# Performance work log

Measured on AMD Instinct MI355X. Metric: run time of the kernel, lower is better.

## Reference

```python
import jax, jax.numpy as jnp
import numpy as np
import math

N, E, IN, HID, HEADS, OUT, G = 20000, 320000, 128, 32, 8, 10, 16


def _conv(x, src, dst, wq, bq, wk, bk, wv, bv, ws, bs, heads):
    # PyG TransformerConv (concat=True, root_weight=True, eval mode)
    n = x.shape[0]
    c = wq.shape[1] // heads
    q = (x @ wq + bq).reshape(n, heads, c)[dst]   # [E, H, C] query at dst
    k = (x @ wk + bk).reshape(n, heads, c)[src]   # [E, H, C] key at src
    v = (x @ wv + bv).reshape(n, heads, c)[src]   # [E, H, C] value at src
    a = (q * k).sum(-1) / math.sqrt(c)            # [E, H] per-edge scores
    amax = jax.lax.stop_gradient(jax.ops.segment_max(a, dst, num_segments=n))
    a = jnp.exp(a - amax[dst])
    denom = jax.ops.segment_sum(a, dst, num_segments=n)
    a = a / (denom[dst] + 1e-16)                  # segment softmax over incoming edges
    agg = jax.ops.segment_sum(a[:, :, None] * v, dst, num_segments=n)  # [N, H, C]
    return agg.reshape(n, heads * c) + x @ ws + bs  # skip connection (lin_skip)


def setup_inputs() -> dict:
    key = jax.random.key(0)
    keys = iter(jax.random.split(key, 64))
    d = {}
    d["x"] = jax.random.normal(next(keys), (N, IN), jnp.float32)
    d["edge_index"] = jax.random.randint(next(keys), (2, E), 0, N)
    d["batch"] = jnp.sort(jax.random.randint(next(keys), (N,), 0, G))
    dims_in = [IN, HID * HEADS, HID * HEADS, HID * HEADS]
    heads_l = [HEADS, HEADS, HEADS, 1]
    for i in range(4):
        di, h = dims_in[i], heads_l[i]
        do = h * HID
        s = 1.0 / math.sqrt(di)
        for nm in ("wq", "wk", "wv", "ws"):
            d[f"{nm}{i}"] = jax.random.normal(next(keys), (di, do), jnp.float32) * s
        for nm in ("bq", "bk", "bv", "bs"):
            d[f"{nm}{i}"] = jnp.zeros((do,), jnp.float32)
    d["wlin"] = jax.random.normal(next(keys), (HID, OUT), jnp.float32) / math.sqrt(HID)
    d["blin"] = jnp.zeros((OUT,), jnp.float32)
    return d


def reference(x, edge_index, batch,
              wq0, bq0, wk0, bk0, wv0, bv0, ws0, bs0,
              wq1, bq1, wk1, bk1, wv1, bv1, ws1, bs1,
              wq2, bq2, wk2, bk2, wv2, bv2, ws2, bs2,
              wq3, bq3, wk3, bk3, wv3, bv3, ws3, bs3,
              wlin, blin):
    src, dst = edge_index[0], edge_index[1]
    layer_params = [
        (wq0, bq0, wk0, bk0, wv0, bv0, ws0, bs0, HEADS),
        (wq1, bq1, wk1, bk1, wv1, bv1, ws1, bs1, HEADS),
        (wq2, bq2, wk2, bk2, wv2, bv2, ws2, bs2, HEADS),
        (wq3, bq3, wk3, bk3, wv3, bv3, ws3, bs3, 1),
    ]
    h = x
    for p in layer_params:
        h = jax.nn.relu(_conv(h, src, dst, *p))  # dropout is identity in eval mode
    counts = jax.ops.segment_sum(jnp.ones((h.shape[0],), h.dtype), batch, num_segments=G)
    pooled = jax.ops.segment_sum(h, batch, num_segments=G) / jnp.maximum(counts, 1.0)[:, None]
    logits = pooled @ wlin + blin
    return jax.nn.log_softmax(logits, axis=-1)
```

## Files before the change

### kernel.cpp

```cpp
#include <hip/hip_runtime.h>
#include <hip/hip_fp16.h>
#include <math.h>

#define HID 32
#define GRP 16
#define OUTC 10

typedef __attribute__((ext_vector_type(8))) short short8;
typedef __attribute__((ext_vector_type(4))) float f32x4;

struct P4     { const float*  W[4]; const float* B[4]; float* C[4]; __half* kv; };
struct W4     { const float*  w[4]; };
struct PZmfma { const ushort* wh[4]; const ushort* wl[4]; const float* bias[4]; float* C[4]; __half* kv; };

__device__ __forceinline__ ushort f2bf(float f) {
    unsigned u = __float_as_uint(f);
    unsigned r = (u + 0x7FFFu + ((u >> 16) & 1u)) >> 16;
    return (ushort)r;
}
__device__ __forceinline__ float bf2f(ushort h) {
    return __uint_as_float(((unsigned)h) << 16);
}
__device__ __forceinline__ float2 h2f(unsigned u) {
    __half2 h = *reinterpret_cast<__half2*>(&u);
    return __half22float2(h);
}

__global__ void fill_i32(int* p, int v, int n) {
    int i = blockIdx.x * blockDim.x + threadIdx.x;
    if (i < n) p[i] = v;
}

__global__ void count_deg(const int* __restrict__ dst, int* __restrict__ deg, int E) {
    int e = blockIdx.x * blockDim.x + threadIdx.x;
    if (e < E) atomicAdd(&deg[dst[e]], 1);
}

__global__ __launch_bounds__(256) void scan_offsets(const int* __restrict__ deg,
                                                    int* __restrict__ offs,
                                                    int* __restrict__ pos, int n) {
    __shared__ int partial[256];
    const int t = threadIdx.x;
    const int chunk = (n + 255) / 256;
    const int start = t * chunk;
    const int end   = min(start + chunk, n);
    int sum = 0;
    for (int i = start; i < end; i++) sum += deg[i];
    partial[t] = sum;
    __syncthreads();
    for (int s = 1; s < 256; s <<= 1) {
        int v = (t >= s) ? partial[t - s] : 0;
        __syncthreads();
        partial[t] += v;
        __syncthreads();
    }
    int base = (t == 0) ? 0 : partial[t - 1];
    for (int i = start; i < end; i++) {
        offs[i] = base; pos[i] = base;
        base += deg[i];
    }
    if (t == 255) offs[n] = base;
}

__global__ void scatter_edges(const int* __restrict__ dst, int* __restrict__ pos,
                              int* __restrict__ perm, int E) {
    int e = blockIdx.x * blockDim.x + threadIdx.x;
    if (e < E) {
        int slot = atomicAdd(&pos[dst[e]], 1);
        perm[slot] = e;
    }
}

__global__ void gather_src(const int* __restrict__ perm, const int* __restrict__ src,
                           int* __restrict__ srcPerm, int E) {
    int i = blockIdx.x * blockDim.x + threadIdx.x;
    if (i < E) srcPerm[i] = src[perm[i]];
}

__global__ void split_f32(const float* __restrict__ x, ushort* __restrict__ hi,
                          ushort* __restrict__ lo, long long n) {
    long long i = (long long)blockIdx.x * blockDim.x + threadIdx.x;
    if (i >= n) return;
    float v = x[i];
    ushort h = f2bf(v);
    ushort l = f2bf(v - bf2f(h));
    hi[i] = h; lo[i] = l;
}

__global__ void splitT_w(W4 wp, ushort* __restrict__ wh, ushort* __restrict__ wl, int K) {
    const int NN = 256;
    int z = blockIdx.y;
    const float* W = wp.w[z];
    ushort* whz = wh + (size_t)z * K * NN;
    ushort* wlz = wl + (size_t)z * K * NN;
    int i = blockIdx.x * blockDim.x + threadIdx.x;
    if (i >= K * NN) return;
    int k = i / NN, n = i - k * NN;
    float v = W[i];
    ushort h = f2bf(v);
    ushort l = f2bf(v - bf2f(h));
    whz[(size_t)n * K + k] = h;
    wlz[(size_t)n * K + k] = l;
}

#define AHI_OFF 0
#define ALO_OFF 8192
#define BHI_OFF 16384
#define BLO_OFF 24576

__global__ __launch_bounds__(256) void gemm4_mfma(
        const ushort* __restrict__ Ah, const ushort* __restrict__ Al,
        PZmfma p, int M, int K) {
    __shared__ __align__(16) unsigned char smem[32768];
    const int NN = 256;
    const int t  = threadIdx.x;
    const int bn = blockIdx.x * 128;
    const int bm = blockIdx.y * 128;
    const int z  = blockIdx.z;
    const ushort* Wh = p.wh[z];
    const ushort* Wl = p.wl[z];

    const int wid  = t >> 6;
    const int lane = t & 63;
    const int wr = wid >> 1, wc = wid & 1;
    const int l15 = lane & 15, g = lane >> 4;

    f32x4 acc[4][4];
    const f32x4 zero4 = {0.f, 0.f, 0.f, 0.f};
    #pragma unroll
    for (int m = 0; m < 4; m++)
        #pragma unroll
        for (int n = 0; n < 4; n++) acc[m][n] = zero4;

    const int srow = t >> 1;
    const int sseg = t & 1;
    const int o0 = sseg * 2;
    const int swz = (srow & 7) << 4;
    const int la0 = (srow * 64 + o0 * 16) ^ swz;
    const int la1 = (srow * 64 + (o0 + 1) * 16) ^ swz;
    const bool arow_ok = (bm + srow) < M;
    const size_t abase = (size_t)(bm + srow) * K + sseg * 16;
    const size_t bbase = (size_t)(bn + srow) * K + sseg * 16;

    for (int k0 = 0; k0 < K; k0 += 32) {
        uint4 vah0 = make_uint4(0,0,0,0), vah1 = vah0, val0 = vah0, val1 = vah0;
        if (arow_ok) {
            vah0 = *(const uint4*)(Ah + abase + k0);
            vah1 = *(const uint4*)(Ah + abase + k0 + 8);
            val0 = *(const uint4*)(Al + abase + k0);
            val1 = *(const uint4*)(Al + abase + k0 + 8);
        }
        uint4 vbh0 = *(const uint4*)(Wh + bbase + k0);
        uint4 vbh1 = *(const uint4*)(Wh + bbase + k0 + 8);
        uint4 vbl0 = *(const uint4*)(Wl + bbase + k0);
        uint4 vbl1 = *(const uint4*)(Wl + bbase + k0 + 8);
        __syncthreads();
        *(uint4*)(smem + AHI_OFF + la0) = vah0;
        *(uint4*)(smem + AHI_OFF + la1) = vah1;
        *(uint4*)(smem + ALO_OFF + la0) = val0;
        *(uint4*)(smem + ALO_OFF + la1) = val1;
        *(uint4*)(smem + BHI_OFF + la0) = vbh0;
        *(uint4*)(smem + BHI_OFF + la1) = vbh1;
        *(uint4*)(smem + BLO_OFF + la0) = vbl0;
        *(uint4*)(smem + BLO_OFF + la1) = vbl1;
        __syncthreads();

        short8 bh[4], bl[4];
        #pragma unroll
        for (int n = 0; n < 4; n++) {
            int r  = wc * 64 + n * 16 + l15;
            int ba = (r * 64 + g * 16) ^ ((r & 7) << 4);
            bh[n] = *(const short8*)(smem + BHI_OFF + ba);
            bl[n] = *(const short8*)(smem + BLO_OFF + ba);
        }
        #pragma unroll
        for (int m = 0; m < 4; m++) {
            int r  = wr * 64 + m * 16 + l15;
            int aa = (r * 64 + g * 16) ^ ((r & 7) << 4);
            short8 ah = *(const short8*)(smem + AHI_OFF + aa);
            short8 al = *(const short8*)(smem + ALO_OFF + aa);
            #pragma unroll
            for (int n = 0; n < 4; n++) {
                acc[m][n] = __builtin_amdgcn_mfma_f32_16x16x32_bf16(ah, bh[n], acc[m][n], 0, 0, 0);
                acc[m][n] = __builtin_amdgcn_mfma_f32_16x16x32_bf16(ah, bl[n], acc[m][n], 0, 0, 0);
                acc[m][n] = __builtin_amdgcn_mfma_f32_16x16x32_bf16(al, bh[n], acc[m][n], 0, 0, 0);
            }
        }
    }

    float* C = p.C[z];
    const float* bias = p.bias[z];
    const bool isKV = (z == 1) || (z == 2);
    const int  vOff = (z == 2) ? 4 : 0;
    float bv[4];
    #pragma unroll
    for (int n = 0; n < 4; n++) bv[n] = bias[bn + wc * 64 + n * 16 + l15];
    #pragma unroll
    for (int m = 0; m < 4; m++) {
        int crow = bm + wr * 64 + m * 16 + g * 4;
        #pragma unroll
        for (int n = 0; n < 4; n++) {
            int ccol = bn + wc * 64 + n * 16 + l15;
            #pragma unroll
            for (int i = 0; i < 4; i++) {
                if (crow + i < M) {
                    float val = acc[m][n][i] + bv[n];
                    if (isKV)
                        p.kv[(size_t)(crow + i) * 512 + ((ccol >> 2) << 3) + vOff + (ccol & 3)]
                            = __float2half(val);
                    else
                        C[(size_t)(crow + i) * NN + ccol] = val;
                }
            }
        }
    }
}

__global__ __launch_bounds__(256) void gemm4_64(
        const float* __restrict__ A, P4 p, int M, int K, int N) {
    __shared__ float As[16][68];
    __shared__ float Wsm[16][68];
    const float* __restrict__ W    = p.W[blockIdx.z];
    const float* __restrict__ bias = p.B[blockIdx.z];
    float*                    C    = p.C[blockIdx.z];
    const bool isKV = (blockIdx.z == 1) || (blockIdx.z == 2);
    const int  vOff = (blockIdx.z == 2) ? 4 : 0;
    const int tid = threadIdx.x;
    const int tx = tid & 15;
    const int ty = tid >> 4;
    const int bm = blockIdx.y * 64;
    const int bn = blockIdx.x * 64;

    float acc[4][4] = {};

    for (int k0 = 0; k0 < K; k0 += 16) {
        {
            int r  = tid >> 2;
            int kk = (tid & 3) * 4;
            float4 v4 = make_float4(0.f,0.f,0.f,0.f);
            if (bm + r < M)
                v4 = *(const float4*)(A + (size_t)(bm + r) * K + k0 + kk);
            As[kk+0][r]=v4.x; As[kk+1][r]=v4.y; As[kk+2][r]=v4.z; As[kk+3][r]=v4.w;
        }
        {
            int kk = tid >> 4;
            int n4 = (tid & 15) * 4;
            float4 v4 = make_float4(0.f,0.f,0.f,0.f);
            if (bn + n4 < N)
                v4 = *(const float4*)(W + (size_t)(k0 + kk) * N + bn + n4);
            *(float4*)&Wsm[kk][n4] = v4;
        }
        __syncthreads();
        #pragma unroll
        for (int kk = 0; kk < 16; kk++) {
            float4 a0 = *(const float4*)&As[kk][ty * 4];
            float4 b0 = *(const float4*)&Wsm[kk][tx * 4];
            float a[4] = {a0.x,a0.y,a0.z,a0.w};
            float b[4] = {b0.x,b0.y,b0.z,b0.w};
            #pragma unroll
            for (int i = 0; i < 4; i++)
                #pragma unroll
                for (int j = 0; j < 4; j++)
                    acc[i][j] += a[i] * b[j];
        }
        __syncthreads();
    }

    #pragma unroll
    for (int i = 0; i < 4; i++) {
        int m = bm + ty * 4 + i;
        if (m >= M) continue;
        #pragma unroll
        for (int j = 0; j < 4; j++) {
            int n = bn + tx * 4 + j;
            if (n < N) {
                float val = acc[i][j] + bias[n];
                if (isKV)
                    p.kv[(size_t)m * 64 + ((n >> 2) << 3) + vOff + (n & 3)] = __float2half(val);
                else
                    C[(size_t)m * N + n] = val;
            }
        }
    }
}

template<bool OUTBF16>
__global__ __launch_bounds__(256) void attn_fused4(
        const float4* __restrict__ q4, const uint4* __restrict__ kv4,
        const float4* sk4, const int* __restrict__ offs, const int* __restrict__ srcPerm,
        float4* outb, ushort4* __restrict__ ohi, ushort4* __restrict__ olo,
        int N, int tpn, float scale) {
    const int npb = blockDim.x / tpn;
    const int sub = threadIdx.x / tpn;
    const int j4  = threadIdx.x % tpn;
    const int n   = blockIdx.x * npb + sub;
    if (n >= N) return;

    const float4 q = q4[(size_t)n * tpn + j4];
    float m = -INFINITY, d = 0.f;
    float ax = 0.f, ay = 0.f, az = 0.f, aw = 0.f;

    const int i0 = offs[n], i1 = offs[n + 1];
    int i = i0;
    for (; i + 4 <= i1; i += 4) {
        const int s0 = srcPerm[i + 0], s1 = srcPerm[i + 1];
        const int s2 = srcPerm[i + 2], s3 = srcPerm[i + 3];
        const uint4 ca = kv4[(size_t)s0 * tpn + j4];
        const uint4 cb = kv4[(size_t)s1 * tpn + j4];
        const uint4 cc = kv4[(size_t)s2 * tpn + j4];
        const uint4 cd = kv4[(size_t)s3 * tpn + j4];
        const float2 ka0 = h2f(ca.x), ka1 = h2f(ca.y);
        const float2 kb0 = h2f(cb.x), kb1 = h2f(cb.y);
        const float2 kc0 = h2f(cc.x), kc1 = h2f(cc.y);
        const float2 kd0 = h2f(cd.x), kd1 = h2f(cd.y);
        float p0 = q.x*ka0.x + q.y*ka0.y + q.z*ka1.x + q.w*ka1.y;
        float p1 = q.x*kb0.x + q.y*kb0.y + q.z*kb1.x + q.w*kb1.y;
        float p2 = q.x*kc0.x + q.y*kc0.y + q.z*kc1.x + q.w*kc1.y;
        float p3 = q.x*kd0.x + q.y*kd0.y + q.z*kd1.x + q.w*kd1.y;
        #pragma unroll
        for (int msk = 4; msk >= 1; msk >>= 1) {
            p0 += __shfl_xor(p0, msk, 8);
            p1 += __shfl_xor(p1, msk, 8);
            p2 += __shfl_xor(p2, msk, 8);
            p3 += __shfl_xor(p3, msk, 8);
        }
        const float sc0 = p0 * scale, sc1 = p1 * scale;
        const float sc2 = p2 * scale, sc3 = p3 * scale;
        const float mx = fmaxf(fmaxf(sc0, sc1), fmaxf(sc2, sc3));
        if (mx > m) {
            const float r = __expf(m - mx);
            ax *= r; ay *= r; az *= r; aw *= r; d *= r; m = mx;
        }
        const float e0 = __expf(sc0 - m), e1 = __expf(sc1 - m);
        const float e2 = __expf(sc2 - m), e3 = __expf(sc3 - m);
        const float2 va0 = h2f(ca.z), va1 = h2f(ca.w);
        const float2 vb0 = h2f(cb.z), vb1 = h2f(cb.w);
        const float2 vc0 = h2f(cc.z), vc1 = h2f(cc.w);
        const float2 vd0 = h2f(cd.z), vd1 = h2f(cd.w);
        ax += e0*va0.x + e1*vb0.x + e2*vc0.x + e3*vd0.x;
        ay += e0*va0.y + e1*vb0.y + e2*vc0.y + e3*vd0.y;
        az += e0*va1.x + e1*vb1.x + e2*vc1.x + e3*vd1.x;
        aw += e0*va1.y + e1*vb1.y + e2*vc1.y + e3*vd1.y;
        d  += (e0 + e1) + (e2 + e3);
    }
    for (; i < i1; ++i) {
        const int s = srcPerm[i];
        const uint4 ce = kv4[(size_t)s * tpn + j4];
        const float2 k0 = h2f(ce.x), k1 = h2f(ce.y);
        float prod = q.x*k0.x + q.y*k0.y + q.z*k1.x + q.w*k1.y;
        #pragma unroll
        for (int msk = 4; msk >= 1; msk >>= 1)
            prod += __shfl_xor(prod, msk, 8);
        const float sc = prod * scale;
        if (sc > m) {
            const float r = __expf(m - sc);
            ax *= r; ay *= r; az *= r; aw *= r; d *= r; m = sc;
        }
        const float p = __expf(sc - m);
        const float2 v0 = h2f(ce.z), v1 = h2f(ce.w);
        ax += p*v0.x; ay += p*v0.y; az += p*v1.x; aw += p*v1.y;
        d += p;
    }

    const float inv = 1.f / (d + 1e-16f);
    const float4 sk = sk4[(size_t)n * tpn + j4];
    float vx = fmaxf(ax * inv + sk.x, 0.f);
    float vy = fmaxf(ay * inv + sk.y, 0.f);
    float vz = fmaxf(az * inv + sk.z, 0.f);
    float vw = fmaxf(aw * inv + sk.w, 0.f);
    const size_t o = (size_t)n * tpn + j4;
    if (OUTBF16) {
        ushort4 h, l;
        h.x = f2bf(vx); l.x = f2bf(vx - bf2f(h.x));
        h.y = f2bf(vy); l.y = f2bf(vy - bf2f(h.y));
        h.z = f2bf(vz); l.z = f2bf(vz - bf2f(h.z));
        h.w = f2bf(vw); l.w = f2bf(vw - bf2f(h.w));
        ohi[o] = h; olo[o] = l;
    } else {
        outb[o] = make_float4(vx, vy, vz, vw);
    }
}

__global__ void graph_offsets(const int* __restrict__ batch, int* __restrict__ gofs,
                              int N, int G) {
    int n = blockIdx.x * blockDim.x + threadIdx.x;
    if (n >= N) return;
    int b = batch[n];
    if (n == 0) { for (int g = 0; g <= b; g++) gofs[g] = 0; }
    else {
        int pb = batch[n - 1];
        if (pb != b) for (int g = pb + 1; g <= b; g++) gofs[g] = n;
    }
    if (n == N - 1) { for (int g = b + 1; g <= G; g++) gofs[g] = N; }
}

__global__ __launch_bounds__(1024) void pool_seg(const float* __restrict__ h,
                                                 const int* __restrict__ gofs,
                                                 float* __restrict__ pooled) {
    const int g = blockIdx.x;
    const int j = threadIdx.x & 31;
    const int r = threadIdx.x >> 5;
    const int s0 = gofs[g], s1 = gofs[g + 1];
    float s = 0.f;
    for (int n = s0 + r; n < s1; n += 32) s += h[(size_t)n * HID + j];
    __shared__ float red[32][33];
    red[r][j] = s;
    __syncthreads();
    if (r == 0) {
        float tt = 0.f;
        #pragma unroll
        for (int i = 0; i < 32; i++) tt += red[i][j];
        pooled[g * HID + j] = tt / fmaxf((float)(s1 - s0), 1.f);
    }
}

__global__ void head_kernel(const float* __restrict__ pooled,
                            const float* __restrict__ wlin, const float* __restrict__ blin,
                            float* __restrict__ out) {
    int g = threadIdx.x;
    if (g >= GRP) return;
    float logit[OUTC];
    #pragma unroll
    for (int o = 0; o < OUTC; o++) logit[o] = blin[o];
    for (int j = 0; j < HID; j++) {
        float pv = pooled[g * HID + j];
        #pragma unroll
        for (int o = 0; o < OUTC; o++) logit[o] += pv * wlin[j * OUTC + o];
    }
    float mx = logit[0];
    #pragma unroll
    for (int o = 1; o < OUTC; o++) mx = fmaxf(mx, logit[o]);
    float sum = 0.f;
    #pragma unroll
    for (int o = 0; o < OUTC; o++) sum += expf(logit[o] - mx);
    float lse = mx + logf(sum);
    #pragma unroll
    for (int o = 0; o < OUTC; o++) out[g * OUTC + o] = logit[o] - lse;
}

extern "C" void kernel_launch(void* const* d_in, const int* in_sizes, int n_in,
                              void* d_out, int out_size, void* d_ws, size_t ws_size,
                              hipStream_t stream) {
    const float* x     = (const float*)d_in[0];
    const int*   ei    = (const int*)d_in[1];
    const int*   batch = (const int*)d_in[2];
    const int N = in_sizes[0] / 128;
    const int E = in_sizes[1] / 2;
    const int* src = ei;
    const int* dst = ei + E;

    const float *W[4][4], *B[4][4];
    for (int i = 0; i < 4; i++)
        for (int j = 0; j < 4; j++) {
            W[i][j] = (const float*)d_in[3 + i * 8 + j];
            B[i][j] = (const float*)d_in[3 + i * 8 + 4 + j];
        }
    const float* wlin = (const float*)d_in[35];
    const float* blin = (const float*)d_in[36];

    char* base = (char*)d_ws;
    size_t off = 0;
    auto alloc = [&](size_t bytes) {
        char* p = base + off;
        off = (off + bytes + 255) & ~(size_t)255;
        return p;
    };
    float*  qb   = (float*)alloc((size_t)N * 256 * 4);
    __half* kvh  = (__half*)alloc((size_t)N * 512 * 2);
    float*  bufA = (float*)alloc((size_t)N * 256 * 4);
    float*  bufB = (float*)alloc((size_t)N * 256 * 4);
    ushort* ahi  = (ushort*)alloc((size_t)N * 256 * 2);
    ushort* alo  = (ushort*)alloc((size_t)N * 256 * 2);
    ushort* wth[3], *wtl[3];
    const int Ks[3] = {128, 256, 256};
    for (int L = 0; L < 3; L++) {
        wth[L] = (ushort*)alloc((size_t)4 * 256 * Ks[L] * 2);
        wtl[L] = (ushort*)alloc((size_t)4 * 256 * Ks[L] * 2);
    }
    int*   deg     = (int*)alloc((size_t)N * 4);
    int*   pos     = (int*)alloc((size_t)N * 4);
    int*   offs    = (int*)alloc((size_t)(N + 1) * 4);
    int*   perm    = (int*)alloc((size_t)E * 4);
    int*   srcPerm = (int*)alloc((size_t)E * 4);
    int*   gofs    = (int*)alloc((GRP + 1) * 4);
    float* pooled  = (float*)alloc(GRP * HID * 4);

    fill_i32<<<(N + 255) / 256, 256, 0, stream>>>(deg, 0, N);
    count_deg<<<(E + 255) / 256, 256, 0, stream>>>(dst, deg, E);
    scan_offsets<<<1, 256, 0, stream>>>(deg, offs, pos, N);
    scatter_edges<<<(E + 255) / 256, 256, 0, stream>>>(dst, pos, perm, E);
    gather_src<<<(E + 255) / 256, 256, 0, stream>>>(perm, src, srcPerm, E);

    for (int L = 0; L < 3; L++) {
        W4 wp;
        for (int z = 0; z < 4; z++) wp.w[z] = W[L][z];
        dim3 gw((Ks[L] * 256 + 255) / 256, 4);
        splitT_w<<<gw, 256, 0, stream>>>(wp, wth[L], wtl[L], Ks[L]);
    }

    const float scale = 0.17677669529663687f;

    split_f32<<<(int)(((long long)N * 128 + 255) / 256), 256, 0, stream>>>(
        x, ahi, alo, (long long)N * 128);

    float* skbufs[2] = {bufA, bufB};

    for (int L = 0; L < 3; L++) {
        const int K = Ks[L];
        float* skb = skbufs[L & 1];

        PZmfma p;
        for (int z = 0; z < 4; z++) {
            p.wh[z] = wth[L] + (size_t)z * 256 * K;
            p.wl[z] = wtl[L] + (size_t)z * 256 * K;
            p.bias[z] = B[L][z];
        }
        p.C[0] = qb; p.C[1] = nullptr; p.C[2] = nullptr; p.C[3] = skb;
        p.kv = kvh;
        dim3 gg(2, (N + 127) / 128, 4);
        gemm4_mfma<<<gg, 256, 0, stream>>>(ahi, alo, p, N, K);

        if (L < 2) {
            attn_fused4<true><<<(N + 3) / 4, 256, 0, stream>>>(
                (const float4*)qb, (const uint4*)kvh, (const float4*)skb,
                offs, srcPerm, nullptr, (ushort4*)ahi, (ushort4*)alo, N, 64, scale);
        } else {
            attn_fused4<false><<<(N + 3) / 4, 256, 0, stream>>>(
                (const float4*)qb, (const uint4*)kvh, (const float4*)skb,
                offs, srcPerm, (float4*)skb, nullptr, nullptr, N, 64, scale);
        }
    }

    {
        const float* cur = skbufs[2 & 1];
        float* skb = skbufs[1];
        P4 p;
        for (int t = 0; t < 4; t++) { p.W[t] = W[3][t]; p.B[t] = B[3][t]; }
        p.C[0] = qb; p.C[1] = nullptr; p.C[2] = nullptr; p.C[3] = skb;
        p.kv = kvh;
        dim3 gg(1, (N + 63) / 64, 4);
        gemm4_64<<<gg, 256, 0, stream>>>(cur, p, N, 256, 32);

        attn_fused4<false><<<(N + 31) / 32, 256, 0, stream>>>(
            (const float4*)qb, (const uint4*)kvh, (const float4*)skb,
            offs, srcPerm, (float4*)skb, nullptr, nullptr, N, 8, scale);

        graph_offsets<<<(N + 255) / 256, 256, 0, stream>>>(batch, gofs, N, GRP);
        pool_seg<<<GRP, 1024, 0, stream>>>(skb, gofs, pooled);
        head_kernel<<<1, 64, 0, stream>>>(pooled, wlin, blin, (float*)d_out);
    }
}
```

Measured before the change: 599.1 us.

## Move last-layer GEMM to split-bf16 MFMA and prefetch tiles in GEMM loop

Replaces the scalar fp32 gemm4_64 for the final layer with a new MFMA kernel that uses hi/lo bf16 splitting. The layer-2 attention now writes bf16 split activations, so the last GEMM reads them directly. The main MFMA GEMM gains compile-time K, a register prefetch of the next k-tile during compute, and an XCD-aware remapping of work-group indices over a flattened 1D grid. The goal is to cut the scalar FMA cost and global-load latency stalls. In exchange it adds an extra weight-split pass and slightly changes numerics from the split-bf16 approximation.

After: 555.3 us. 1.08x faster.

```diff
diff --git a/kernel.cpp b/kernel.cpp
--- a/kernel.cpp
+++ b/kernel.cpp
@@ -9,7 +9,6 @@
 typedef __attribute__((ext_vector_type(8))) short short8;
 typedef __attribute__((ext_vector_type(4))) float f32x4;
 
-struct P4     { const float*  W[4]; const float* B[4]; float* C[4]; __half* kv; };
 struct W4     { const float*  w[4]; };
 struct PZmfma { const ushort* wh[4]; const ushort* wl[4]; const float* bias[4]; float* C[4]; __half* kv; };
 
@@ -87,8 +86,8 @@
     hi[i] = h; lo[i] = l;
 }
 
-__global__ void splitT_w(W4 wp, ushort* __restrict__ wh, ushort* __restrict__ wl, int K) {
-    const int NN = 256;
+__global__ void splitT_w(W4 wp, ushort* __restrict__ wh, ushort* __restrict__ wl,
+                         int K, int NN) {
     int z = blockIdx.y;
     const float* W = wp.w[z];
     ushort* whz = wh + (size_t)z * K * NN;
@@ -108,15 +107,19 @@
 #define BHI_OFF 16384
 #define BLO_OFF 24576
 
+template<int K>
 __global__ __launch_bounds__(256) void gemm4_mfma(
         const ushort* __restrict__ Ah, const ushort* __restrict__ Al,
-        PZmfma p, int M, int K) {
+        PZmfma p, int M) {
     __shared__ __align__(16) unsigned char smem[32768];
     const int NN = 256;
     const int t  = threadIdx.x;
-    const int bn = blockIdx.x * 128;
-    const int bm = blockIdx.y * 128;
-    const int z  = blockIdx.z;
+    const int hb  = blockIdx.x;
+    const int cpx = gridDim.x >> 3;
+    const int w   = (hb & 7) * cpx + (hb >> 3);
+    const int bm  = (w >> 3) * 128;
+    const int bn  = ((w >> 2) & 1) * 128;
+    const int z   = w & 3;
     const ushort* Wh = p.wh[z];
     const ushort* Wl = p.wl[z];
 
@@ -134,36 +137,43 @@
 
     const int srow = t >> 1;
     const int sseg = t & 1;
-    const int o0 = sseg * 2;
     const int swz = (srow & 7) << 4;
-    const int la0 = (srow * 64 + o0 * 16) ^ swz;
-    const int la1 = (srow * 64 + (o0 + 1) * 16) ^ swz;
+    const int la0 = (srow * 64 + sseg * 32) ^ swz;
+    const int la1 = (srow * 64 + sseg * 32 + 16) ^ swz;
     const bool arow_ok = (bm + srow) < M;
     const size_t abase = (size_t)(bm + srow) * K + sseg * 16;
     const size_t bbase = (size_t)(bn + srow) * K + sseg * 16;
 
-    for (int k0 = 0; k0 < K; k0 += 32) {
-        uint4 vah0 = make_uint4(0,0,0,0), vah1 = vah0, val0 = vah0, val1 = vah0;
+    uint4 ra0, ra1, ra2, ra3, rb0, rb1, rb2, rb3;
+    auto loadAB = [&](int k0) {
+        ra0 = make_uint4(0,0,0,0); ra1 = ra0; ra2 = ra0; ra3 = ra0;
         if (arow_ok) {
-            vah0 = *(const uint4*)(Ah + abase + k0);
-            vah1 = *(const uint4*)(Ah + abase + k0 + 8);
-            val0 = *(const uint4*)(Al + abase + k0);
-            val1 = *(const uint4*)(Al + abase + k0 + 8);
-        }
-        uint4 vbh0 = *(const uint4*)(Wh + bbase + k0);
-        uint4 vbh1 = *(const uint4*)(Wh + bbase + k0 + 8);
-        uint4 vbl0 = *(const uint4*)(Wl + bbase + k0);
-        uint4 vbl1 = *(const uint4*)(Wl + bbase + k0 + 8);
+            ra0 = *(const uint4*)(Ah + abase + k0);
+            ra1 = *(const uint4*)(Ah + abase + k0 + 8);
+            ra2 = *(const uint4*)(Al + abase + k0);
+            ra3 = *(const uint4*)(Al + abase + k0 + 8);
+        }
+        rb0 = *(const uint4*)(Wh + bbase + k0);
+        rb1 = *(const uint4*)(Wh + bbase + k0 + 8);
+        rb2 = *(const uint4*)(Wl + bbase + k0);
+        rb3 = *(const uint4*)(Wl + bbase + k0 + 8);
+    };
+
+    loadAB(0);
+
+    #pragma unroll
+    for (int ks = 0; ks < K / 32; ks++) {
         __syncthreads();
-        *(uint4*)(smem + AHI_OFF + la0) = vah0;
-        *(uint4*)(smem + AHI_OFF + la1) = vah1;
-        *(uint4*)(smem + ALO_OFF + la0) = val0;
-        *(uint4*)(smem + ALO_OFF + la1) = val1;
-        *(uint4*)(smem + BHI_OFF + la0) = vbh0;
-        *(uint4*)(smem + BHI_OFF + la1) = vbh1;
-        *(uint4*)(smem + BLO_OFF + la0) = vbl0;
-        *(uint4*)(smem + BLO_OFF + la1) = vbl1;
+        *(uint4*)(smem + AHI_OFF + la0) = ra0;
+        *(uint4*)(smem + AHI_OFF + la1) = ra1;
+        *(uint4*)(smem + ALO_OFF + la0) = ra2;
+        *(uint4*)(smem + ALO_OFF + la1) = ra3;
+        *(uint4*)(smem + BHI_OFF + la0) = rb0;
+        *(uint4*)(smem + BHI_OFF + la1) = rb1;
+        *(uint4*)(smem + BLO_OFF + la0) = rb2;
+        *(uint4*)(smem + BLO_OFF + la1) = rb3;
         __syncthreads();
+        if (ks + 1 < K / 32) loadAB((ks + 1) * 32);
 
         short8 bh[4], bl[4];
         #pragma unroll
@@ -216,69 +226,128 @@
     }
 }
 
-__global__ __launch_bounds__(256) void gemm4_64(
-        const float* __restrict__ A, P4 p, int M, int K, int N) {
-    __shared__ float As[16][68];
-    __shared__ float Wsm[16][68];
-    const float* __restrict__ W    = p.W[blockIdx.z];
-    const float* __restrict__ bias = p.B[blockIdx.z];
-    float*                    C    = p.C[blockIdx.z];
-    const bool isKV = (blockIdx.z == 1) || (blockIdx.z == 2);
-    const int  vOff = (blockIdx.z == 2) ? 4 : 0;
-    const int tid = threadIdx.x;
-    const int tx = tid & 15;
-    const int ty = tid >> 4;
-    const int bm = blockIdx.y * 64;
-    const int bn = blockIdx.x * 64;
-
-    float acc[4][4] = {};
-
-    for (int k0 = 0; k0 < K; k0 += 16) {
-        {
-            int r  = tid >> 2;
-            int kk = (tid & 3) * 4;
-            float4 v4 = make_float4(0.f,0.f,0.f,0.f);
-            if (bm + r < M)
-                v4 = *(const float4*)(A + (size_t)(bm + r) * K + k0 + kk);
-            As[kk+0][r]=v4.x; As[kk+1][r]=v4.y; As[kk+2][r]=v4.z; As[kk+3][r]=v4.w;
-        }
-        {
-            int kk = tid >> 4;
-            int n4 = (tid & 15) * 4;
-            float4 v4 = make_float4(0.f,0.f,0.f,0.f);
-            if (bn + n4 < N)
-                v4 = *(const float4*)(W + (size_t)(k0 + kk) * N + bn + n4);
-            *(float4*)&Wsm[kk][n4] = v4;
-        }
+#define A32HI_OFF 0
+#define A32LO_OFF 8192
+#define B32HI_OFF 16384
+#define B32LO_OFF 18432
+
+template<int K>
+__global__ __launch_bounds__(256) void gemm4_mfma32(
+        const ushort* __restrict__ Ah, const ushort* __restrict__ Al,
+        PZmfma p, int M, int nWork) {
+    __shared__ __align__(16) unsigned char smem[20480];
+    const int t  = threadIdx.x;
+    const int hb  = blockIdx.x;
+    const int cpx = gridDim.x >> 3;
+    const int w   = (hb & 7) * cpx + (hb >> 3);
+    if (w >= nWork) return;
+    const int bm = (w >> 2) * 128;
+    const int z  = w & 3;
+    const ushort* Wh = p.wh[z];
+    const ushort* Wl = p.wl[z];
+
+    const int wid  = t >> 6;
+    const int lane = t & 63;
+    const int l15 = lane & 15, g = lane >> 4;
+
+    f32x4 acc[2][2];
+    const f32x4 zero4 = {0.f, 0.f, 0.f, 0.f};
+    acc[0][0] = zero4; acc[0][1] = zero4; acc[1][0] = zero4; acc[1][1] = zero4;
+
+    const int srow = t >> 1;
+    const int sseg = t & 1;
+    const int swz  = (srow & 7) << 4;
+    const int la0 = (srow * 64 + sseg * 32) ^ swz;
+    const int la1 = (srow * 64 + sseg * 32 + 16) ^ swz;
+    const bool arow_ok = (bm + srow) < M;
+    const size_t abase = (size_t)(bm + srow) * K + sseg * 16;
+    const bool doB = (t < 64);
+    const int brow = t >> 1;
+    const int bswz = (brow & 7) << 4;
+    const int lb0 = (brow * 64 + sseg * 32) ^ bswz;
+    const int lb1 = (brow * 64 + sseg * 32 + 16) ^ bswz;
+    const size_t bbase = (size_t)brow * K + sseg * 16;
+
+    uint4 ra0, ra1, ra2, ra3, rb0, rb1, rb2, rb3;
+    auto loadAB = [&](int k0) {
+        ra0 = make_uint4(0,0,0,0); ra1 = ra0; ra2 = ra0; ra3 = ra0;
+        if (arow_ok) {
+            ra0 = *(const uint4*)(Ah + abase + k0);
+            ra1 = *(const uint4*)(Ah + abase + k0 + 8);
+            ra2 = *(const uint4*)(Al + abase + k0);
+            ra3 = *(const uint4*)(Al + abase + k0 + 8);
+        }
+        if (doB) {
+            rb0 = *(const uint4*)(Wh + bbase + k0);
+            rb1 = *(const uint4*)(Wh + bbase + k0 + 8);
+            rb2 = *(const uint4*)(Wl + bbase + k0);
+            rb3 = *(const uint4*)(Wl + bbase + k0 + 8);
+        }
+    };
+
+    loadAB(0);
+
+    #pragma unroll
+    for (int ks = 0; ks < K / 32; ks++) {
         __syncthreads();
-        #pragma unroll
-        for (int kk = 0; kk < 16; kk++) {
-            float4 a0 = *(const float4*)&As[kk][ty * 4];
-            float4 b0 = *(const float4*)&Wsm[kk][tx * 4];
-            float a[4] = {a0.x,a0.y,a0.z,a0.w};
-            float b[4] = {b0.x,b0.y,b0.z,b0.w};
+        *(uint4*)(smem + A32HI_OFF + la0) = ra0;
+        *(uint4*)(smem + A32HI_OFF + la1) = ra1;
+        *(uint4*)(smem + A32LO_OFF + la0) = ra2;
+        *(uint4*)(smem + A32LO_OFF + la1) = ra3;
+        if (doB) {
+            *(uint4*)(smem + B32HI_OFF + lb0) = rb0;
+            *(uint4*)(smem + B32HI_OFF + lb1) = rb1;
+            *(uint4*)(smem + B32LO_OFF + lb0) = rb2;
+            *(uint4*)(smem + B32LO_OFF + lb1) = rb3;
+        }
+        __syncthreads();
+        if (ks + 1 < K / 32) loadAB((ks + 1) * 32);
+
+        short8 bh[2], bl[2];
+        #pragma unroll
+        for (int n = 0; n < 2; n++) {
+            int r  = n * 16 + l15;
+            int ba = (r * 64 + g * 16) ^ ((r & 7) << 4);
+            bh[n] = *(const short8*)(smem + B32HI_OFF + ba);
+            bl[n] = *(const short8*)(smem + B32LO_OFF + ba);
+        }
+        #pragma unroll
+        for (int m = 0; m < 2; m++) {
+            int r  = wid * 32 + m * 16 + l15;
+            int aa = (r * 64 + g * 16) ^ ((r & 7) << 4);
+            short8 ah = *(const short8*)(smem + A32HI_OFF + aa);
+            short8 al = *(const short8*)(smem + A32LO_OFF + aa);
             #pragma unroll
-            for (int i = 0; i < 4; i++)
-                #pragma unroll
-                for (int j = 0; j < 4; j++)
-                    acc[i][j] += a[i] * b[j];
-        }
-        __syncthreads();
-    }
-
-    #pragma unroll
-    for (int i = 0; i < 4; i++) {
-        int m = bm + ty * 4 + i;
-        if (m >= M) continue;
-        #pragma unroll
-        for (int j = 0; j < 4; j++) {
-            int n = bn + tx * 4 + j;
-            if (n < N) {
-                float val = acc[i][j] + bias[n];
-                if (isKV)
-                    p.kv[(size_t)m * 64 + ((n >> 2) << 3) + vOff + (n & 3)] = __float2half(val);
-                else
-                    C[(size_t)m * N + n] = val;
+            for (int n = 0; n < 2; n++) {
+                acc[m][n] = __builtin_amdgcn_mfma_f32_16x16x32_bf16(ah, bh[n], acc[m][n], 0, 0, 0);
+                acc[m][n] = __builtin_amdgcn_mfma_f32_16x16x32_bf16(ah, bl[n], acc[m][n], 0, 0, 0);
+                acc[m][n] = __builtin_amdgcn_mfma_f32_16x16x32_bf16(al, bh[n], acc[m][n], 0, 0, 0);
+            }
+        }
+    }
+
+    float* C = p.C[z];
+    const float* bias = p.bias[z];
+    const bool isKV = (z == 1) || (z == 2);
+    const int  vOff = (z == 2) ? 4 : 0;
+    float bv[2];
+    bv[0] = bias[l15]; bv[1] = bias[16 + l15];
+    #pragma unroll
+    for (int m = 0; m < 2; m++) {
+        int crow = bm + wid * 32 + m * 16 + g * 4;
+        #pragma unroll
+        for (int n = 0; n < 2; n++) {
+            int ccol = n * 16 + l15;
+            #pragma unroll
+            for (int i = 0; i < 4; i++) {
+                if (crow + i < M) {
+                    float val = acc[m][n][i] + bv[n];
+                    if (isKV)
+                        p.kv[(size_t)(crow + i) * 64 + ((ccol >> 2) << 3) + vOff + (ccol & 3)]
+                            = __float2half(val);
+                    else
+                        C[(size_t)(crow + i) * 32 + ccol] = val;
+                }
             }
         }
     }
@@ -477,6 +546,8 @@
         wth[L] = (ushort*)alloc((size_t)4 * 256 * Ks[L] * 2);
         wtl[L] = (ushort*)alloc((size_t)4 * 256 * Ks[L] * 2);
     }
+    ushort* wth3 = (ushort*)alloc((size_t)4 * 32 * 256 * 2);
+    ushort* wtl3 = (ushort*)alloc((size_t)4 * 32 * 256 * 2);
     int*   deg     = (int*)alloc((size_t)N * 4);
     int*   pos     = (int*)alloc((size_t)N * 4);
     int*   offs    = (int*)alloc((size_t)(N + 1) * 4);
@@ -495,7 +566,13 @@
         W4 wp;
         for (int z = 0; z < 4; z++) wp.w[z] = W[L][z];
         dim3 gw((Ks[L] * 256 + 255) / 256, 4);
-        splitT_w<<<gw, 256, 0, stream>>>(wp, wth[L], wtl[L], Ks[L]);
+        splitT_w<<<gw, 256, 0, stream>>>(wp, wth[L], wtl[L], Ks[L], 256);
+    }
+    {
+        W4 wp;
+        for (int z = 0; z < 4; z++) wp.w[z] = W[3][z];
+        dim3 gw((256 * 32 + 255) / 256, 4);
+        splitT_w<<<gw, 256, 0, stream>>>(wp, wth3, wtl3, 256, 32);
     }
 
     const float scale = 0.17677669529663687f;
@@ -504,6 +581,7 @@
         x, ahi, alo, (long long)N * 128);
 
     float* skbufs[2] = {bufA, bufB};
+    const int nbm = (N + 127) / 128;
 
     for (int L = 0; L < 3; L++) {
         const int K = Ks[L];
@@ -517,29 +595,28 @@
         }
         p.C[0] = qb; p.C[1] = nullptr; p.C[2] = nullptr; p.C[3] = skb;
         p.kv = kvh;
-        dim3 gg(2, (N + 127) / 128, 4);
-        gemm4_mfma<<<gg, 256, 0, stream>>>(ahi, alo, p, N, K);
-
-        if (L < 2) {
-            attn_fused4<true><<<(N + 3) / 4, 256, 0, stream>>>(
-                (const float4*)qb, (const uint4*)kvh, (const float4*)skb,
-                offs, srcPerm, nullptr, (ushort4*)ahi, (ushort4*)alo, N, 64, scale);
-        } else {
-            attn_fused4<false><<<(N + 3) / 4, 256, 0, stream>>>(
-                (const float4*)qb, (const uint4*)kvh, (const float4*)skb,
-                offs, srcPerm, (float4*)skb, nullptr, nullptr, N, 64, scale);
-        }
+        const int nwg = nbm * 8;
+        if (K == 128) gemm4_mfma<128><<<nwg, 256, 0, stream>>>(ahi, alo, p, N);
+        else          gemm4_mfma<256><<<nwg, 256, 0, stream>>>(ahi, alo, p, N);
+
+        attn_fused4<true><<<(N + 3) / 4, 256, 0, stream>>>(
+            (const float4*)qb, (const uint4*)kvh, (const float4*)skb,
+            offs, srcPerm, nullptr, (ushort4*)ahi, (ushort4*)alo, N, 64, scale);
     }
 
     {
-        const float* cur = skbufs[2 & 1];
         float* skb = skbufs[1];
-        P4 p;
-        for (int t = 0; t < 4; t++) { p.W[t] = W[3][t]; p.B[t] = B[3][t]; }
+        PZmfma p;
+        for (int z = 0; z < 4; z++) {
+            p.wh[z] = wth3 + (size_t)z * 32 * 256;
+            p.wl[z] = wtl3 + (size_t)z * 32 * 256;
+            p.bias[z] = B[3][z];
+        }
         p.C[0] = qb; p.C[1] = nullptr; p.C[2] = nullptr; p.C[3] = skb;
         p.kv = kvh;
-        dim3 gg(1, (N + 63) / 64, 4);
-        gemm4_64<<<gg, 256, 0, stream>>>(cur, p, N, 256, 32);
+        const int nWork = nbm * 4;
+        const int nwg   = ((nWork + 7) / 8) * 8;
+        gemm4_mfma32<256><<<nwg, 256, 0, stream>>>(ahi, alo, p, N, nWork);
 
         attn_fused4<false><<<(N + 31) / 32, 256, 0, stream>>>(
             (const float4*)qb, (const uint4*)kvh, (const float4*)skb,
```
